# Kernel optimization log

Hardware: AMD Instinct MI355X
Metric: run time of the kernel (lower is better)

Reference implementation:

```python
import jax, jax.numpy as jnp
import numpy as np

B, C, H, W = 1, 1, 1024, 1024
NP = 16                    # n_patches
S = NP * NP                # 256 tokens
D = 2048                   # hidden_d
NH = 16                    # heads
DH = D // NH               # 128
MLP = 4 * D
NB = 2                     # blocks
INPUT_D = C * (H // NP) * (W // NP)  # 4096
EPS = 1e-5


def positional_embeddings(s, d):
    # result[i,j] = sin(i/10000**(j/d)) if j even else cos(i/10000**((j-1)/d))
    i = jnp.arange(s, dtype=jnp.float32)[:, None]
    j = jnp.arange(d, dtype=jnp.float32)[None, :]
    even = (jnp.arange(d) % 2 == 0)[None, :]
    expo = jnp.where(even, j, j - 1.0) / d
    ang = i / (10000.0 ** expo)
    return jnp.where(even, jnp.sin(ang), jnp.cos(ang))


def layer_norm(x, g, b):
    m = x.mean(-1, keepdims=True)
    v = ((x - m) ** 2).mean(-1, keepdims=True)
    return (x - m) / jnp.sqrt(v + EPS) * g + b


def setup_inputs() -> dict:
    key = jax.random.key(0)
    ks = jax.random.split(key, 20)
    s = 0.02
    return {
        "images": jax.random.normal(ks[0], (B, C, H, W), jnp.float32),
        "memory": jax.random.normal(ks[1], (1, 8), jnp.float32),
        "wmap": jax.random.normal(ks[2], (INPUT_D, D), jnp.float32) * s,
        "bmap": jnp.zeros((D,), jnp.float32),
        "ln1_g": jnp.ones((NB, D), jnp.float32),
        "ln1_b": jnp.zeros((NB, D), jnp.float32),
        "qw": jax.random.normal(ks[3], (NB, NH, DH, DH), jnp.float32) * s,
        "qb": jnp.zeros((NB, NH, DH), jnp.float32),
        "kw": jax.random.normal(ks[4], (NB, NH, DH, DH), jnp.float32) * s,
        "kb": jnp.zeros((NB, NH, DH), jnp.float32),
        "vw": jax.random.normal(ks[5], (NB, NH, DH, DH), jnp.float32) * s,
        "vb": jnp.zeros((NB, NH, DH), jnp.float32),
        "ln2_g": jnp.ones((NB, D), jnp.float32),
        "ln2_b": jnp.zeros((NB, D), jnp.float32),
        "w1": jax.random.normal(ks[6], (NB, D, MLP), jnp.float32) * s,
        "b1": jnp.zeros((NB, MLP), jnp.float32),
        "w2": jax.random.normal(ks[7], (NB, MLP, D), jnp.float32) * s,
        "b2": jnp.zeros((NB, D), jnp.float32),
        "head_w": jax.random.normal(ks[8], (D, 1), jnp.float32) * s,
        "head_b": jnp.zeros((1,), jnp.float32),
    }


def reference(images, memory, wmap, bmap, ln1_g, ln1_b, qw, qb, kw, kb, vw, vb,
              ln2_g, ln2_b, w1, b1, w2, b2, head_w, head_b):
    # patchify: view(1, n_patches**2, num_h*num_v) -> (1, 256, 4096)
    patches = images.reshape(1, S, INPUT_D)
    tokens = patches @ wmap + bmap                      # (1, S, D)
    x = tokens + positional_embeddings(S, D)
    scale = DH ** 0.5
    for l in range(NB):
        h = layer_norm(x, ln1_g[l], ln1_b[l])
        h4 = h.reshape(B, S, NH, DH)
        q = jnp.einsum('bshd,hde->bshe', h4, qw[l]) + qb[l]
        k = jnp.einsum('bshd,hde->bshe', h4, kw[l]) + kb[l]
        v = jnp.einsum('bshd,hde->bshe', h4, vw[l]) + vb[l]
        att = jax.nn.softmax(jnp.einsum('bshe,bthe->bhst', q, k) / scale, axis=-1)
        attn_out = jnp.einsum('bhst,bthe->bshe', att, v).reshape(B, S, D)
        x = x + attn_out
        h2 = layer_norm(x, ln2_g[l], ln2_b[l])
        x = x + (jax.nn.gelu(h2 @ w1[l] + b1[l], approximate=False) @ w2[l] + b2[l])
    cls = x[:, 0]                                       # (1, D)
    out = jax.nn.sigmoid(cls @ head_w + head_b)         # (1, 1)
    return (out, memory)
```

## Files before the change

### kernel.cpp

```cpp
#include <hip/hip_runtime.h>
#include <math.h>

#define SQ   256
#define DD   2048
#define NHD  16
#define DHD  128
#define MLPD 8192
#define KIN  4096
#define INV_SQRT_DH 0.08838834764831845f

typedef __attribute__((ext_vector_type(8))) short bf16x8;
typedef __attribute__((ext_vector_type(4))) float f32x4;

__device__ __forceinline__ float gelu_f(float x) {
    return 0.5f * x * (1.0f + erff(x * 0.70710678118654752f));
}

__device__ __forceinline__ short f2bf(float f) {
    unsigned u = __float_as_uint(f);
    unsigned r = (u + 0x7fffu + ((u >> 16) & 1u)) >> 16;
    return (short)r;
}

__global__ __launch_bounds__(512) void gemm128(const float* __restrict__ A,
                                               const float* __restrict__ W,
                                               float* __restrict__ C,
                                               int N, int K, int KC) {
    __shared__ short As[2][128 * 64];
    __shared__ short Bs[2][128 * 64];
    const int tid = threadIdx.x;
    const int n0 = blockIdx.x * 128, m0 = blockIdx.y * 128;
    const int kstart = blockIdx.z * KC;
    const int ln = tid & 63;
    const int wv = tid >> 6;
    const int l15 = ln & 15, q = ln >> 4;
    const int wm = wv >> 2, wn = wv & 3;

    f32x4 acc[4][2];
    #pragma unroll
    for (int mt = 0; mt < 4; mt++)
        #pragma unroll
        for (int nt = 0; nt < 2; nt++) acc[mt][nt] = (f32x4){0.f, 0.f, 0.f, 0.f};

    const int am = tid >> 2, ak0 = (tid & 3) * 16;
    const int bn = tid & 127, bk0 = (tid >> 7) * 16;
    const int aw0 = am * 64 + ((((ak0 >> 3) + 0) ^ (am & 7)) * 8);
    const int aw1 = am * 64 + ((((ak0 >> 3) + 1) ^ (am & 7)) * 8);
    const int bw0 = bn * 64 + ((((bk0 >> 3) + 0) ^ (bn & 7)) * 8);
    const int bw1 = bn * 64 + ((((bk0 >> 3) + 1) ^ (bn & 7)) * 8);

    const float* aptr = A + (size_t)(m0 + am) * K + kstart + ak0;
    const float* wptr = W + (size_t)(kstart + bk0) * N + n0 + bn;

    const int nch = KC >> 6;

    float4 a[4];
    float wb[16];
    #pragma unroll
    for (int j = 0; j < 4; j++) a[j] = *(const float4*)(aptr + 4 * j);
    #pragma unroll
    for (int j = 0; j < 16; j++) wb[j] = wptr[(size_t)j * N];
    {
        short t0[16];
        #pragma unroll
        for (int j = 0; j < 4; j++) {
            t0[4 * j]     = f2bf(a[j].x);
            t0[4 * j + 1] = f2bf(a[j].y);
            t0[4 * j + 2] = f2bf(a[j].z);
            t0[4 * j + 3] = f2bf(a[j].w);
        }
        *(bf16x8*)&As[0][aw0] = *(bf16x8*)&t0[0];
        *(bf16x8*)&As[0][aw1] = *(bf16x8*)&t0[8];
        short u0[16];
        #pragma unroll
        for (int j = 0; j < 16; j++) u0[j] = f2bf(wb[j]);
        *(bf16x8*)&Bs[0][bw0] = *(bf16x8*)&u0[0];
        *(bf16x8*)&Bs[0][bw1] = *(bf16x8*)&u0[8];
    }
    __syncthreads();

    int cur = 0;
    for (int t = 0; t < nch; t++) {
        const bool pf = (t + 1 < nch);
        if (pf) {
            const float* ap = aptr + (t + 1) * 64;
            #pragma unroll
            for (int j = 0; j < 4; j++) a[j] = *(const float4*)(ap + 4 * j);
            const float* wp = wptr + (size_t)(t + 1) * 64 * N;
            #pragma unroll
            for (int j = 0; j < 16; j++) wb[j] = wp[(size_t)j * N];
        }

        const short* Ab = As[cur];
        const short* Bb = Bs[cur];
        bf16x8 af[4][2], bf[2][2];
        #pragma unroll
        for (int mt = 0; mt < 4; mt++) {
            const int ar = wm * 64 + mt * 16 + l15;
            af[mt][0] = *(const bf16x8*)&Ab[ar * 64 + ((q ^ (ar & 7)) * 8)];
            af[mt][1] = *(const bf16x8*)&Ab[ar * 64 + (((q + 4) ^ (ar & 7)) * 8)];
        }
        #pragma unroll
        for (int nt = 0; nt < 2; nt++) {
            const int br = wn * 32 + nt * 16 + l15;
            bf[nt][0] = *(const bf16x8*)&Bb[br * 64 + ((q ^ (br & 7)) * 8)];
            bf[nt][1] = *(const bf16x8*)&Bb[br * 64 + (((q + 4) ^ (br & 7)) * 8)];
        }
        #pragma unroll
        for (int mt = 0; mt < 4; mt++)
            #pragma unroll
            for (int nt = 0; nt < 2; nt++) {
                acc[mt][nt] = __builtin_amdgcn_mfma_f32_16x16x32_bf16(af[mt][0], bf[nt][0], acc[mt][nt], 0, 0, 0);
                acc[mt][nt] = __builtin_amdgcn_mfma_f32_16x16x32_bf16(af[mt][1], bf[nt][1], acc[mt][nt], 0, 0, 0);
            }

        if (pf) {
            short t1[16];
            #pragma unroll
            for (int j = 0; j < 4; j++) {
                t1[4 * j]     = f2bf(a[j].x);
                t1[4 * j + 1] = f2bf(a[j].y);
                t1[4 * j + 2] = f2bf(a[j].z);
                t1[4 * j + 3] = f2bf(a[j].w);
            }
            short* Aw = (short*)As[cur ^ 1];
            short* Bw = (short*)Bs[cur ^ 1];
            *(bf16x8*)&Aw[aw0] = *(bf16x8*)&t1[0];
            *(bf16x8*)&Aw[aw1] = *(bf16x8*)&t1[8];
            short u1[16];
            #pragma unroll
            for (int j = 0; j < 16; j++) u1[j] = f2bf(wb[j]);
            *(bf16x8*)&Bw[bw0] = *(bf16x8*)&u1[0];
            *(bf16x8*)&Bw[bw1] = *(bf16x8*)&u1[8];
        }
        __syncthreads();
        cur ^= 1;
    }

    #pragma unroll
    for (int mt = 0; mt < 4; mt++) {
        #pragma unroll
        for (int nt = 0; nt < 2; nt++) {
            const int col = n0 + wn * 32 + nt * 16 + l15;
            #pragma unroll
            for (int i = 0; i < 4; i++) {
                const int row = m0 + wm * 64 + mt * 16 + q * 4 + i;
                atomicAdd(&C[(size_t)row * N + col], acc[mt][nt][i]);
            }
        }
    }
}

__global__ __launch_bounds__(256) void epi_pos(float* __restrict__ x,
                                               const float* __restrict__ bmap) {
    const int idx = blockIdx.x * 256 + threadIdx.x;
    const int m = idx >> 11, n = idx & 2047;
    float val = x[idx] + bmap[n];
    float jf = (float)n;
    float expo = ((n & 1) ? (jf - 1.0f) : jf) * (1.0f / 2048.0f);
    float ang = (float)m * powf(10000.0f, -expo);
    x[idx] = val + ((n & 1) ? cosf(ang) : sinf(ang));
}

__global__ __launch_bounds__(256) void epi_gelu(float* __restrict__ y,
                                                const float* __restrict__ b1) {
    const int idx = blockIdx.x * 256 + threadIdx.x;
    y[idx] = gelu_f(y[idx] + b1[idx & 8191]);
}

__global__ __launch_bounds__(256) void epi_bias(float* __restrict__ x,
                                                const float* __restrict__ b2) {
    const int idx = blockIdx.x * 256 + threadIdx.x;
    x[idx] += b2[idx & 2047];
}

__global__ __launch_bounds__(256) void qkv_mfma(const float* __restrict__ h,
                                                const float* __restrict__ qw, const float* __restrict__ kw,
                                                const float* __restrict__ vw, const float* __restrict__ qb,
                                                const float* __restrict__ kb, const float* __restrict__ vb,
                                                float* __restrict__ q, float* __restrict__ k,
                                                float* __restrict__ v) {
    __shared__ short As[64 * 64];
    __shared__ short Bs[64 * 64];
    const int head = blockIdx.x, m0 = blockIdx.y * 64;
    const int type = blockIdx.z >> 1, n0 = (blockIdx.z & 1) * 64;
    const float* W; const float* B; float* O;
    if (type == 0)      { W = qw; B = qb; O = q; }
    else if (type == 1) { W = kw; B = kb; O = k; }
    else                { W = vw; B = vb; O = v; }
    W += (size_t)head * DHD * DHD;
    B += head * DHD;
    const int hoff = head * DHD;
    const int tid = threadIdx.x;
    const int wv = tid >> 6, ln = tid & 63;
    const int l15 = ln & 15, qq = ln >> 4;

    f32x4 acc[4];
    #pragma unroll
    for (int j = 0; j < 4; j++) acc[j] = (f32x4){0.f, 0.f, 0.f, 0.f};

    const int am = tid >> 2, akb = (tid & 3) * 16, ac0 = (tid & 3) * 2;
    const int bn = tid & 63, bkb = (tid >> 6) * 16, bc0 = (tid >> 6) * 2;
    short* as0 = &As[am * 64 + ((ac0 ^ (am & 7)) * 8)];
    short* as1 = &As[am * 64 + (((ac0 + 1) ^ (am & 7)) * 8)];
    short* bs0 = &Bs[bn * 64 + ((bc0 ^ (bn & 7)) * 8)];
    short* bs1 = &Bs[bn * 64 + (((bc0 + 1) ^ (bn & 7)) * 8)];
    const int arow = 16 * wv + l15;
    const short* af0 = &As[arow * 64 + ((qq ^ (arow & 7)) * 8)];
    const short* af1 = &As[arow * 64 + (((qq + 4) ^ (arow & 7)) * 8)];

    for (int kc = 0; kc < DHD; kc += 64) {
        const float* ap = h + (size_t)(m0 + am) * DD + hoff + kc + akb;
        float4 a0 = *(const float4*)ap;
        float4 a1 = *(const float4*)(ap + 4);
        float4 a2 = *(const float4*)(ap + 8);
        float4 a3 = *(const float4*)(ap + 12);
        const float* wp = W + (size_t)(kc + bkb) * DHD + n0 + bn;
        float wb[16];
        #pragma unroll
        for (int j = 0; j < 16; j++) wb[j] = wp[j * DHD];

        __syncthreads();
        {
            short t[16] = {f2bf(a0.x), f2bf(a0.y), f2bf(a0.z), f2bf(a0.w),
                           f2bf(a1.x), f2bf(a1.y), f2bf(a1.z), f2bf(a1.w),
                           f2bf(a2.x), f2bf(a2.y), f2bf(a2.z), f2bf(a2.w),
                           f2bf(a3.x), f2bf(a3.y), f2bf(a3.z), f2bf(a3.w)};
            *(bf16x8*)as0 = *(bf16x8*)&t[0];
            *(bf16x8*)as1 = *(bf16x8*)&t[8];
            short u[16];
            #pragma unroll
            for (int j = 0; j < 16; j++) u[j] = f2bf(wb[j]);
            *(bf16x8*)bs0 = *(bf16x8*)&u[0];
            *(bf16x8*)bs1 = *(bf16x8*)&u[8];
        }
        __syncthreads();

        bf16x8 fa0 = *(const bf16x8*)af0;
        bf16x8 fa1 = *(const bf16x8*)af1;
        #pragma unroll
        for (int jt = 0; jt < 4; jt++) {
            const int brow = 16 * jt + l15;
            bf16x8 fb0 = *(const bf16x8*)&Bs[brow * 64 + ((qq ^ (brow & 7)) * 8)];
            bf16x8 fb1 = *(const bf16x8*)&Bs[brow * 64 + (((qq + 4) ^ (brow & 7)) * 8)];
            acc[jt] = __builtin_amdgcn_mfma_f32_16x16x32_bf16(fa0, fb0, acc[jt], 0, 0, 0);
            acc[jt] = __builtin_amdgcn_mfma_f32_16x16x32_bf16(fa1, fb1, acc[jt], 0, 0, 0);
        }
    }
    #pragma unroll
    for (int jt = 0; jt < 4; jt++) {
        const int n = n0 + 16 * jt + l15;
        #pragma unroll
        for (int i = 0; i < 4; i++) {
            const int m = m0 + 16 * wv + qq * 4 + i;
            O[(size_t)m * DD + hoff + n] = acc[jt][i] + B[n];
        }
    }
}

__global__ __launch_bounds__(256) void attn_mfma(const float* __restrict__ q,
                                                 const float* __restrict__ k,
                                                 const float* __restrict__ v,
                                                 float* __restrict__ x) {
    __shared__ short P[64 * 272];
    __shared__ short ST[9216];
    const int head = blockIdx.y, r0 = blockIdx.x * 64;
    const int hoff = head * DHD;
    const int tid = threadIdx.x;
    const int wv = tid >> 6, ln = tid & 63;
    const int l15 = ln & 15, qd = ln >> 4;

    bf16x8 af[4];
    {
        const float* qp = q + (size_t)(r0 + 16 * wv + l15) * DD + hoff + qd * 8;
        #pragma unroll
        for (int s = 0; s < 4; s++) {
            float4 f0 = *(const float4*)(qp + s * 32);
            float4 f1 = *(const float4*)(qp + s * 32 + 4);
            short t[8] = {f2bf(f0.x), f2bf(f0.y), f2bf(f0.z), f2bf(f0.w),
                          f2bf(f1.x), f2bf(f1.y), f2bf(f1.z), f2bf(f1.w)};
            af[s] = *(bf16x8*)t;
        }
    }

    f32x4 sacc[16];
    #pragma unroll
    for (int i = 0; i < 16; i++) sacc[i] = (f32x4){0.f, 0.f, 0.f, 0.f};

    const int skey = tid >> 2, scol = (tid & 3) * 32;
    for (int kq = 0; kq < 4; kq++) {
        const float* kp = k + (size_t)(kq * 64 + skey) * DD + hoff + scol;
        float4 f[8];
        #pragma unroll
        for (int a = 0; a < 8; a++) f[a] = *(const float4*)(kp + a * 4);
        if (kq) __syncthreads();
        #pragma unroll
        for (int a = 0; a < 4; a++) {
            short t[8] = {f2bf(f[2*a].x), f2bf(f[2*a].y), f2bf(f[2*a].z), f2bf(f[2*a].w),
                          f2bf(f[2*a+1].x), f2bf(f[2*a+1].y), f2bf(f[2*a+1].z), f2bf(f[2*a+1].w)};
            *(bf16x8*)&ST[skey * 136 + scol + a * 8] = *(bf16x8*)t;
        }
        __syncthreads();
        #pragma unroll
        for (int nl = 0; nl < 4; nl++) {
            #pragma unroll
            for (int s = 0; s < 4; s++) {
                bf16x8 bfr = *(const bf16x8*)&ST[(nl * 16 + l15) * 136 + s * 32 + qd * 8];
                sacc[kq * 4 + nl] = __builtin_amdgcn_mfma_f32_16x16x32_bf16(af[s], bfr, sacc[kq * 4 + nl], 0, 0, 0);
            }
        }
    }

    float inv_s[4];
    #pragma unroll
    for (int i = 0; i < 4; i++) {
        float m = -1e30f;
        #pragma unroll
        for (int nt = 0; nt < 16; nt++) m = fmaxf(m, sacc[nt][i]);
        m = fmaxf(m, __shfl_xor(m, 1));
        m = fmaxf(m, __shfl_xor(m, 2));
        m = fmaxf(m, __shfl_xor(m, 4));
        m = fmaxf(m, __shfl_xor(m, 8));
        float sum = 0.f;
        #pragma unroll
        for (int nt = 0; nt < 16; nt++) {
            float e = __expf((sacc[nt][i] - m) * INV_SQRT_DH);
            sacc[nt][i] = e;
            sum += e;
        }
        sum += __shfl_xor(sum, 1);
        sum += __shfl_xor(sum, 2);
        sum += __shfl_xor(sum, 4);
        sum += __shfl_xor(sum, 8);
        inv_s[i] = 1.0f / sum;
    }
    #pragma unroll
    for (int nt = 0; nt < 16; nt++) {
        const int col = nt * 16 + l15;
        const int chunk = col >> 3, c7 = col & 7;
        #pragma unroll
        for (int i = 0; i < 4; i++) {
            const int row = 16 * wv + 4 * qd + i;
            P[row * 272 + ((chunk ^ (row & 7)) * 8) + c7] = f2bf(sacc[nt][i] * inv_s[i]);
        }
    }
    __syncthreads();

    f32x4 oacc[8];
    #pragma unroll
    for (int e = 0; e < 8; e++) oacc[e] = (f32x4){0.f, 0.f, 0.f, 0.f};

    const int ve = tid & 127, vks = (tid >> 7) * 32;
    for (int kq = 0; kq < 4; kq++) {
        float vv[32];
        #pragma unroll
        for (int j = 0; j < 32; j++)
            vv[j] = v[(size_t)(kq * 64 + vks + j) * DD + hoff + ve];
        if (kq) __syncthreads();
        #pragma unroll
        for (int c = 0; c < 4; c++) {
            short t[8];
            #pragma unroll
            for (int b = 0; b < 8; b++) t[b] = f2bf(vv[c * 8 + b]);
            const int ch = (vks >> 3) + c;
            *(bf16x8*)&ST[ve * 72 + ((ch ^ (ve & 7)) * 8)] = *(bf16x8*)t;
        }
        __syncthreads();
        #pragma unroll
        for (int s = 0; s < 2; s++) {
            const int row = 16 * wv + l15;
            const int pc = kq * 8 + s * 4 + qd;
            bf16x8 pa = *(const bf16x8*)&P[row * 272 + ((pc ^ (row & 7)) * 8)];
            #pragma unroll
            for (int et = 0; et < 8; et++) {
                const int er = et * 16 + l15;
                const int vc = s * 4 + qd;
                bf16x8 vb = *(const bf16x8*)&ST[er * 72 + ((vc ^ (er & 7)) * 8)];
                oacc[et] = __builtin_amdgcn_mfma_f32_16x16x32_bf16(pa, vb, oacc[et], 0, 0, 0);
            }
        }
    }
    #pragma unroll
    for (int et = 0; et < 8; et++) {
        const int e = et * 16 + l15;
        #pragma unroll
        for (int i = 0; i < 4; i++) {
            const int row = r0 + 16 * wv + 4 * qd + i;
            x[(size_t)row * DD + hoff + e] += oacc[et][i];
        }
    }
}

__global__ __launch_bounds__(256) void ln_kernel(const float* __restrict__ xin,
                                                 const float* __restrict__ g,
                                                 const float* __restrict__ b,
                                                 float* __restrict__ out,
                                                 float* __restrict__ zbuf, int zn) {
    __shared__ float red[8];
    const int tid = threadIdx.x;
    for (int i = tid; i < zn; i += 256) zbuf[i] = 0.0f;
    const int row = blockIdx.x;
    const float* xr = xin + row * DD;
    float vals[8];
    float s = 0.0f;
    #pragma unroll
    for (int i = 0; i < 8; i++) { vals[i] = xr[tid + i * 256]; s += vals[i]; }
    #pragma unroll
    for (int o = 32; o > 0; o >>= 1) s += __shfl_down(s, o);
    if ((tid & 63) == 0) red[tid >> 6] = s;
    __syncthreads();
    if (tid == 0) red[4] = (red[0] + red[1] + red[2] + red[3]) * (1.0f / 2048.0f);
    __syncthreads();
    const float mean = red[4];
    float vs = 0.0f;
    #pragma unroll
    for (int i = 0; i < 8; i++) { float d = vals[i] - mean; vs += d * d; }
    #pragma unroll
    for (int o = 32; o > 0; o >>= 1) vs += __shfl_down(vs, o);
    if ((tid & 63) == 0) red[tid >> 6] = vs;
    __syncthreads();
    if (tid == 0) red[5] = rsqrtf((red[0] + red[1] + red[2] + red[3]) * (1.0f / 2048.0f) + 1e-5f);
    __syncthreads();
    const float inv = red[5];
    #pragma unroll
    for (int i = 0; i < 8; i++) {
        int c = tid + i * 256;
        out[row * DD + c] = (vals[i] - mean) * inv * g[c] + b[c];
    }
}

__global__ __launch_bounds__(256) void attn0_kernel(const float* __restrict__ q,
                                                    const float* __restrict__ k,
                                                    const float* __restrict__ v,
                                                    float* __restrict__ x) {
    __shared__ float q0[128];
    __shared__ float p[256];
    __shared__ float red[8];
    const int h = blockIdx.x, tid = threadIdx.x, hoff = h * DHD;
    if (tid < 128) q0[tid] = q[hoff + tid];
    __syncthreads();
    const float* kr = k + tid * DD + hoff;
    float s = 0.0f;
    #pragma unroll 8
    for (int d = 0; d < 128; d++) s += q0[d] * kr[d];
    s *= INV_SQRT_DH;
    float m = s;
    #pragma unroll
    for (int o = 32; o > 0; o >>= 1) m = fmaxf(m, __shfl_down(m, o));
    if ((tid & 63) == 0) red[tid >> 6] = m;
    __syncthreads();
    if (tid == 0) red[4] = fmaxf(fmaxf(red[0], red[1]), fmaxf(red[2], red[3]));
    __syncthreads();
    const float mx = red[4];
    float e = __expf(s - mx);
    p[tid] = e;
    float t = e;
    #pragma unroll
    for (int o = 32; o > 0; o >>= 1) t += __shfl_down(t, o);
    if ((tid & 63) == 0) red[tid >> 6] = t;
    __syncthreads();
    if (tid == 0) red[5] = red[0] + red[1] + red[2] + red[3];
    __syncthreads();
    const float inv = 1.0f / red[5];
    if (tid < 128) {
        float acc = 0.0f;
        #pragma unroll 8
        for (int j = 0; j < 256; j++) acc += p[j] * v[j * DD + hoff + tid];
        x[hoff + tid] += acc * inv;
    }
}

__global__ __launch_bounds__(256) void gemv1_kernel(const float* __restrict__ h2,
                                                    const float* __restrict__ w1,
                                                    float* __restrict__ y) {
    const int n = blockIdx.x * 256 + threadIdx.x;
    const int k0 = blockIdx.y * 64;
    float s = 0.0f;
    #pragma unroll 8
    for (int k = 0; k < 64; k++) s += h2[k0 + k] * w1[(size_t)(k0 + k) * MLPD + n];
    atomicAdd(&y[n], s);
}

__global__ __launch_bounds__(256) void gelu_bias_kernel(float* __restrict__ y,
                                                        const float* __restrict__ b1) {
    const int n = blockIdx.x * 256 + threadIdx.x;
    y[n] = gelu_f(y[n] + b1[n]);
}

__global__ __launch_bounds__(256) void gemv2_kernel(const float* __restrict__ y1,
                                                    const float* __restrict__ w2,
                                                    float* __restrict__ x) {
    const int m = blockIdx.x * 256 + threadIdx.x;
    const int k0 = blockIdx.y * 256;
    float s = 0.0f;
    #pragma unroll 8
    for (int k = 0; k < 256; k++) s += y1[k0 + k] * w2[(size_t)(k0 + k) * DD + m];
    atomicAdd(&x[m], s);
}

__global__ __launch_bounds__(256) void head_kernel(const float* __restrict__ x,
                                                   const float* __restrict__ b2l,
                                                   const float* __restrict__ hw,
                                                   const float* __restrict__ hb,
                                                   const float* __restrict__ mem,
                                                   float* __restrict__ out) {
    __shared__ float red[8];
    const int tid = threadIdx.x;
    float s = 0.0f;
    for (int m = tid; m < 2048; m += 256) s += (x[m] + b2l[m]) * hw[m];
    #pragma unroll
    for (int o = 32; o > 0; o >>= 1) s += __shfl_down(s, o);
    if ((tid & 63) == 0) red[tid >> 6] = s;
    __syncthreads();
    if (tid == 0) {
        float t = red[0] + red[1] + red[2] + red[3];
        out[0] = 1.0f / (1.0f + __expf(-(t + hb[0])));
    }
    if (tid < 8) out[1 + tid] = mem[tid];
}

extern "C" void kernel_launch(void* const* d_in, const int* in_sizes, int n_in,
                              void* d_out, int out_size, void* d_ws, size_t ws_size,
                              hipStream_t stream) {
    const float* images = (const float*)d_in[0];
    const float* memory = (const float*)d_in[1];
    const float* wmap   = (const float*)d_in[2];
    const float* bmap   = (const float*)d_in[3];
    const float* ln1_g  = (const float*)d_in[4];
    const float* ln1_b  = (const float*)d_in[5];
    const float* qw     = (const float*)d_in[6];
    const float* qb     = (const float*)d_in[7];
    const float* kw     = (const float*)d_in[8];
    const float* kb     = (const float*)d_in[9];
    const float* vw     = (const float*)d_in[10];
    const float* vb     = (const float*)d_in[11];
    const float* ln2_g  = (const float*)d_in[12];
    const float* ln2_b  = (const float*)d_in[13];
    const float* w1     = (const float*)d_in[14];
    const float* b1     = (const float*)d_in[15];
    const float* w2     = (const float*)d_in[16];
    const float* b2     = (const float*)d_in[17];
    const float* head_w = (const float*)d_in[18];
    const float* head_b = (const float*)d_in[19];
    float* out = (float*)d_out;

    float* ws = (float*)d_ws;
    float* x     = ws;
    float* h     = x + SQ * DD;
    float* q     = h + SQ * DD;
    float* k     = q + SQ * DD;
    float* v     = k + SQ * DD;
    float* y1    = v + SQ * DD;
    float* y1row = y1 + SQ * MLPD;
    float* h2row = y1row + MLPD;

    hipMemsetAsync(x, 0, (size_t)SQ * DD * sizeof(float), stream);
    gemm128<<<dim3(DD / 128, SQ / 128, 8), 512, 0, stream>>>(images, wmap, x, DD, KIN, 512);
    epi_pos<<<SQ * DD / 256, 256, 0, stream>>>(x, bmap);

    for (int l = 0; l < 2; l++) {
        const size_t wofs = (size_t)l * NHD * DHD * DHD;
        const size_t bofs = (size_t)l * NHD * DHD;
        ln_kernel<<<SQ, 256, 0, stream>>>(x, ln1_g + l * DD, ln1_b + l * DD, h, nullptr, 0);
        qkv_mfma<<<dim3(NHD, SQ / 64, 6), 256, 0, stream>>>(h, qw + wofs, kw + wofs, vw + wofs,
                                                            qb + bofs, kb + bofs, vb + bofs,
                                                            q, k, v);
        if (l == 0) {
            attn_mfma<<<dim3(SQ / 64, NHD), 256, 0, stream>>>(q, k, v, x);
            ln_kernel<<<SQ, 256, 0, stream>>>(x, ln2_g, ln2_b, h, nullptr, 0);
            hipMemsetAsync(y1, 0, (size_t)SQ * MLPD * sizeof(float), stream);
            gemm128<<<dim3(MLPD / 128, SQ / 128, 2), 512, 0, stream>>>(h, w1, y1, MLPD, DD, 1024);
            epi_gelu<<<SQ * MLPD / 256, 256, 0, stream>>>(y1, b1);
            gemm128<<<dim3(DD / 128, SQ / 128, 8), 512, 0, stream>>>(y1, w2, x, DD, MLPD, 1024);
            epi_bias<<<SQ * DD / 256, 256, 0, stream>>>(x, b2);
        } else {
            attn0_kernel<<<NHD, 256, 0, stream>>>(q, k, v, x);
            ln_kernel<<<1, 256, 0, stream>>>(x, ln2_g + DD, ln2_b + DD, h2row, y1row, MLPD);
            gemv1_kernel<<<dim3(MLPD / 256, 32), 256, 0, stream>>>(h2row, w1 + (size_t)DD * MLPD, y1row);
            gelu_bias_kernel<<<MLPD / 256, 256, 0, stream>>>(y1row, b1 + MLPD);
            gemv2_kernel<<<dim3(DD / 256, 32), 256, 0, stream>>>(y1row, w2 + (size_t)DD * MLPD, x);
            head_kernel<<<1, 256, 0, stream>>>(x, b2 + DD, head_w, head_b, memory, out);
        }
    }
}
```

Measured before the change: 497.7 us.

## Pre-transpose weights to bf16 and stream GEMM tiles via direct global-to-LDS loads

Adds conversion kernels that cast the image to bf16 and transpose wmap, w1 and w2 into K-contiguous bf16 layouts on every call. The GEMM is rewritten as gemm_bf, which loads pre-swizzled 16-byte chunks straight into LDS with global_load_lds, dropping the per-iteration fp32 loads and in-register bf16 conversion. The layer-norm and GELU epilogues now also emit bf16 copies to feed it. The aim is to cut GEMM load and convert overhead and the strided weight reads. The cost is an extra full read and write of roughly 160MB of fp32 weights inside the timed region, which may outweigh the GEMM savings.

Measured after the change: 538.5 us. 1.08x slower.

```diff
diff --git a/kernel.cpp b/kernel.cpp
--- a/kernel.cpp
+++ b/kernel.cpp
@@ -22,8 +22,48 @@
     return (short)r;
 }
 
-__global__ __launch_bounds__(512) void gemm128(const float* __restrict__ A,
-                                               const float* __restrict__ W,
+__device__ __forceinline__ void gload16(const void* g, void* l) {
+    __builtin_amdgcn_global_load_lds((const __attribute__((address_space(1))) void*)g,
+                                     (__attribute__((address_space(3))) void*)l,
+                                     16, 0, 0);
+}
+
+__global__ __launch_bounds__(256) void cvt_bf(const float* __restrict__ in,
+                                              short* __restrict__ out) {
+    const int idx = (blockIdx.x * 256 + threadIdx.x) * 8;
+    float4 f0 = *(const float4*)&in[idx];
+    float4 f1 = *(const float4*)&in[idx + 4];
+    short u[8] = {f2bf(f0.x), f2bf(f0.y), f2bf(f0.z), f2bf(f0.w),
+                  f2bf(f1.x), f2bf(f1.y), f2bf(f1.z), f2bf(f1.w)};
+    *(bf16x8*)&out[idx] = *(bf16x8*)&u[0];
+}
+
+__global__ __launch_bounds__(256) void transpose_bf(const float* __restrict__ in,
+                                                    short* __restrict__ out,
+                                                    int K, int N) {
+    __shared__ float T[64][65];
+    const int k0 = blockIdx.y * 64, n0 = blockIdx.x * 64;
+    const int tid = threadIdx.x;
+    const int kr = tid >> 4, nc = (tid & 15) * 4;
+    #pragma unroll
+    for (int i = 0; i < 4; i++) {
+        float4 f = *(const float4*)&in[(size_t)(k0 + kr + 16 * i) * N + n0 + nc];
+        T[kr + 16 * i][nc]     = f.x;
+        T[kr + 16 * i][nc + 1] = f.y;
+        T[kr + 16 * i][nc + 2] = f.z;
+        T[kr + 16 * i][nc + 3] = f.w;
+    }
+    __syncthreads();
+    const int nr = tid >> 2, kc = (tid & 3) * 16;
+    short u[16];
+    #pragma unroll
+    for (int j = 0; j < 16; j++) u[j] = f2bf(T[kc + j][nr]);
+    *(bf16x8*)&out[(size_t)(n0 + nr) * K + k0 + kc]     = *(bf16x8*)&u[0];
+    *(bf16x8*)&out[(size_t)(n0 + nr) * K + k0 + kc + 8] = *(bf16x8*)&u[8];
+}
+
+__global__ __launch_bounds__(512) void gemm_bf(const short* __restrict__ A,
+                                               const short* __restrict__ Bt,
                                                float* __restrict__ C,
                                                int N, int K, int KC) {
     __shared__ short As[2][128 * 64];
@@ -31,8 +71,7 @@
     const int tid = threadIdx.x;
     const int n0 = blockIdx.x * 128, m0 = blockIdx.y * 128;
     const int kstart = blockIdx.z * KC;
-    const int ln = tid & 63;
-    const int wv = tid >> 6;
+    const int wv = tid >> 6, ln = tid & 63;
     const int l15 = ln & 15, q = ln >> 4;
     const int wm = wv >> 2, wn = wv & 3;
 
@@ -42,57 +81,33 @@
         #pragma unroll
         for (int nt = 0; nt < 2; nt++) acc[mt][nt] = (f32x4){0.f, 0.f, 0.f, 0.f};
 
-    const int am = tid >> 2, ak0 = (tid & 3) * 16;
-    const int bn = tid & 127, bk0 = (tid >> 7) * 16;
-    const int aw0 = am * 64 + ((((ak0 >> 3) + 0) ^ (am & 7)) * 8);
-    const int aw1 = am * 64 + ((((ak0 >> 3) + 1) ^ (am & 7)) * 8);
-    const int bw0 = bn * 64 + ((((bk0 >> 3) + 0) ^ (bn & 7)) * 8);
-    const int bw1 = bn * 64 + ((((bk0 >> 3) + 1) ^ (bn & 7)) * 8);
-
-    const float* aptr = A + (size_t)(m0 + am) * K + kstart + ak0;
-    const float* wptr = W + (size_t)(kstart + bk0) * N + n0 + bn;
+    const int srow = tid >> 3;
+    const int schk = (tid & 7) ^ (srow & 7);
+    const short* Ap = A  + (size_t)(m0 + srow) * K + kstart + schk * 8;
+    const short* Bp = Bt + (size_t)(n0 + srow) * K + kstart + schk * 8;
+    const int wvoff = wv * 1024;
 
     const int nch = KC >> 6;
 
-    float4 a[4];
-    float wb[16];
-    #pragma unroll
-    for (int j = 0; j < 4; j++) a[j] = *(const float4*)(aptr + 4 * j);
-    #pragma unroll
-    for (int j = 0; j < 16; j++) wb[j] = wptr[(size_t)j * N];
-    {
-        short t0[16];
-        #pragma unroll
-        for (int j = 0; j < 4; j++) {
-            t0[4 * j]     = f2bf(a[j].x);
-            t0[4 * j + 1] = f2bf(a[j].y);
-            t0[4 * j + 2] = f2bf(a[j].z);
-            t0[4 * j + 3] = f2bf(a[j].w);
-        }
-        *(bf16x8*)&As[0][aw0] = *(bf16x8*)&t0[0];
-        *(bf16x8*)&As[0][aw1] = *(bf16x8*)&t0[8];
-        short u0[16];
-        #pragma unroll
-        for (int j = 0; j < 16; j++) u0[j] = f2bf(wb[j]);
-        *(bf16x8*)&Bs[0][bw0] = *(bf16x8*)&u0[0];
-        *(bf16x8*)&Bs[0][bw1] = *(bf16x8*)&u0[8];
+    #pragma unroll
+    for (int j = 0; j < 2; j++) {
+        gload16(Ap + (size_t)(j * 64) * K, (char*)(&As[0][0]) + j * 8192 + wvoff);
+        gload16(Bp + (size_t)(j * 64) * K, (char*)(&Bs[0][0]) + j * 8192 + wvoff);
     }
     __syncthreads();
 
     int cur = 0;
     for (int t = 0; t < nch; t++) {
-        const bool pf = (t + 1 < nch);
-        if (pf) {
-            const float* ap = aptr + (t + 1) * 64;
-            #pragma unroll
-            for (int j = 0; j < 4; j++) a[j] = *(const float4*)(ap + 4 * j);
-            const float* wp = wptr + (size_t)(t + 1) * 64 * N;
-            #pragma unroll
-            for (int j = 0; j < 16; j++) wb[j] = wp[(size_t)j * N];
-        }
-
-        const short* Ab = As[cur];
-        const short* Bb = Bs[cur];
+        if (t + 1 < nch) {
+            const int kc = (t + 1) * 64;
+            #pragma unroll
+            for (int j = 0; j < 2; j++) {
+                gload16(Ap + (size_t)(j * 64) * K + kc, (char*)(&As[cur ^ 1][0]) + j * 8192 + wvoff);
+                gload16(Bp + (size_t)(j * 64) * K + kc, (char*)(&Bs[cur ^ 1][0]) + j * 8192 + wvoff);
+            }
+        }
+        const short* Ab = &As[cur][0];
+        const short* Bb = &Bs[cur][0];
         bf16x8 af[4][2], bf[2][2];
         #pragma unroll
         for (int mt = 0; mt < 4; mt++) {
@@ -113,26 +128,6 @@
                 acc[mt][nt] = __builtin_amdgcn_mfma_f32_16x16x32_bf16(af[mt][0], bf[nt][0], acc[mt][nt], 0, 0, 0);
                 acc[mt][nt] = __builtin_amdgcn_mfma_f32_16x16x32_bf16(af[mt][1], bf[nt][1], acc[mt][nt], 0, 0, 0);
             }
-
-        if (pf) {
-            short t1[16];
-            #pragma unroll
-            for (int j = 0; j < 4; j++) {
-                t1[4 * j]     = f2bf(a[j].x);
-                t1[4 * j + 1] = f2bf(a[j].y);
-                t1[4 * j + 2] = f2bf(a[j].z);
-                t1[4 * j + 3] = f2bf(a[j].w);
-            }
-            short* Aw = (short*)As[cur ^ 1];
-            short* Bw = (short*)Bs[cur ^ 1];
-            *(bf16x8*)&Aw[aw0] = *(bf16x8*)&t1[0];
-            *(bf16x8*)&Aw[aw1] = *(bf16x8*)&t1[8];
-            short u1[16];
-            #pragma unroll
-            for (int j = 0; j < 16; j++) u1[j] = f2bf(wb[j]);
-            *(bf16x8*)&Bw[bw0] = *(bf16x8*)&u1[0];
-            *(bf16x8*)&Bw[bw1] = *(bf16x8*)&u1[8];
-        }
         __syncthreads();
         cur ^= 1;
     }
@@ -162,10 +157,11 @@
     x[idx] = val + ((n & 1) ? cosf(ang) : sinf(ang));
 }
 
-__global__ __launch_bounds__(256) void epi_gelu(float* __restrict__ y,
-                                                const float* __restrict__ b1) {
+__global__ __launch_bounds__(256) void epi_gelu(const float* __restrict__ y,
+                                                const float* __restrict__ b1,
+                                                short* __restrict__ yb) {
     const int idx = blockIdx.x * 256 + threadIdx.x;
-    y[idx] = gelu_f(y[idx] + b1[idx & 8191]);
+    yb[idx] = f2bf(gelu_f(y[idx] + b1[idx & 8191]));
 }
 
 __global__ __launch_bounds__(256) void epi_bias(float* __restrict__ x,
@@ -395,7 +391,8 @@
                                                  const float* __restrict__ g,
                                                  const float* __restrict__ b,
                                                  float* __restrict__ out,
-                                                 float* __restrict__ zbuf, int zn) {
+                                                 float* __restrict__ zbuf, int zn,
+                                                 short* __restrict__ out_bf) {
     __shared__ float red[8];
     const int tid = threadIdx.x;
     for (int i = tid; i < zn; i += 256) zbuf[i] = 0.0f;
@@ -425,7 +422,9 @@
     #pragma unroll
     for (int i = 0; i < 8; i++) {
         int c = tid + i * 256;
-        out[row * DD + c] = (vals[i] - mean) * inv * g[c] + b[c];
+        float val = (vals[i] - mean) * inv * g[c] + b[c];
+        out[row * DD + c] = val;
+        if (out_bf) out_bf[row * DD + c] = f2bf(val);
     }
 }
 
@@ -554,28 +553,41 @@
     float* y1row = y1 + SQ * MLPD;
     float* h2row = y1row + MLPD;
 
+    short* sws    = (short*)(h2row + DD);
+    short* img_bf = sws;
+    short* wmapT  = img_bf + (size_t)SQ * KIN;
+    short* w1T    = wmapT + (size_t)DD * KIN;
+    short* w2T    = w1T + (size_t)MLPD * DD;
+    short* h_bf   = w2T + (size_t)DD * MLPD;
+    short* y1b    = h_bf + (size_t)SQ * DD;
+
+    cvt_bf<<<(SQ * KIN) / (256 * 8), 256, 0, stream>>>(images, img_bf);
+    transpose_bf<<<dim3(DD / 64, KIN / 64), 256, 0, stream>>>(wmap, wmapT, KIN, DD);
+    transpose_bf<<<dim3(MLPD / 64, DD / 64), 256, 0, stream>>>(w1, w1T, DD, MLPD);
+    transpose_bf<<<dim3(DD / 64, MLPD / 64), 256, 0, stream>>>(w2, w2T, MLPD, DD);
+
     hipMemsetAsync(x, 0, (size_t)SQ * DD * sizeof(float), stream);
-    gemm128<<<dim3(DD / 128, SQ / 128, 8), 512, 0, stream>>>(images, wmap, x, DD, KIN, 512);
+    gemm_bf<<<dim3(DD / 128, SQ / 128, 8), 512, 0, stream>>>(img_bf, wmapT, x, DD, KIN, 512);
     epi_pos<<<SQ * DD / 256, 256, 0, stream>>>(x, bmap);
 
     for (int l = 0; l < 2; l++) {
         const size_t wofs = (size_t)l * NHD * DHD * DHD;
         const size_t bofs = (size_t)l * NHD * DHD;
-        ln_kernel<<<SQ, 256, 0, stream>>>(x, ln1_g + l * DD, ln1_b + l * DD, h, nullptr, 0);
+        ln_kernel<<<SQ, 256, 0, stream>>>(x, ln1_g + l * DD, ln1_b + l * DD, h, nullptr, 0, nullptr);
         qkv_mfma<<<dim3(NHD, SQ / 64, 6), 256, 0, stream>>>(h, qw + wofs, kw + wofs, vw + wofs,
                                                             qb + bofs, kb + bofs, vb + bofs,
                                                             q, k, v);
         if (l == 0) {
             attn_mfma<<<dim3(SQ / 64, NHD), 256, 0, stream>>>(q, k, v, x);
-            ln_kernel<<<SQ, 256, 0, stream>>>(x, ln2_g, ln2_b, h, nullptr, 0);
+            ln_kernel<<<SQ, 256, 0, stream>>>(x, ln2_g, ln2_b, h, nullptr, 0, h_bf);
             hipMemsetAsync(y1, 0, (size_t)SQ * MLPD * sizeof(float), stream);
-            gemm128<<<dim3(MLPD / 128, SQ / 128, 2), 512, 0, stream>>>(h, w1, y1, MLPD, DD, 1024);
-            epi_gelu<<<SQ * MLPD / 256, 256, 0, stream>>>(y1, b1);
-            gemm128<<<dim3(DD / 128, SQ / 128, 8), 512, 0, stream>>>(y1, w2, x, DD, MLPD, 1024);
+            gemm_bf<<<dim3(MLPD / 128, SQ / 128, 2), 512, 0, stream>>>(h_bf, w1T, y1, MLPD, DD, 1024);
+            epi_gelu<<<SQ * MLPD / 256, 256, 0, stream>>>(y1, b1, y1b);
+            gemm_bf<<<dim3(DD / 128, SQ / 128, 8), 512, 0, stream>>>(y1b, w2T, x, DD, MLPD, 1024);
             epi_bias<<<SQ * DD / 256, 256, 0, stream>>>(x, b2);
         } else {
             attn0_kernel<<<NHD, 256, 0, stream>>>(q, k, v, x);
-            ln_kernel<<<1, 256, 0, stream>>>(x, ln2_g + DD, ln2_b + DD, h2row, y1row, MLPD);
+            ln_kernel<<<1, 256, 0, stream>>>(x, ln2_g + DD, ln2_b + DD, h2row, y1row, MLPD, nullptr);
             gemv1_kernel<<<dim3(MLPD / 256, 32), 256, 0, stream>>>(h2row, w1 + (size_t)DD * MLPD, y1row);
             gelu_bias_kernel<<<MLPD / 256, 256, 0, stream>>>(y1row, b1 + MLPD);
             gemv2_kernel<<<dim3(DD / 256, 32), 256, 0, stream>>>(y1row, w2 + (size_t)DD * MLPD, x);
```

## Fuse GEMM epilogues, drop split-K memsets, fuse LN into GEMV path

Applied to the files above, without the earlier changes.

Templates the bf16 MFMA GEMM with three epilogue modes. Mode 0 adds the bias and positional embedding, mode 1 applies bias plus GELU, and both write directly with split-K removed. Mode 2 keeps atomic split-K for the MLP down-projection, now with 4 splits. This removes the memsets of x and y1 and the separate elementwise epilogue kernels. The b2 bias add moves into the next layer-norm. In the single-row second layer, the LN is fused into gemv1 (each block recomputes the LN) and GELU into gemv2. Dropping split-K on the first two GEMMs gives fewer blocks (32 and 128 CTAs), which may under-fill the GPU and lengthen the serial K loop.

New measurement: 612.0 us. 1.23x slower.

```diff
diff --git a/kernel.cpp b/kernel.cpp
--- a/kernel.cpp
+++ b/kernel.cpp
@@ -8,6 +8,7 @@
 #define MLPD 8192
 #define KIN  4096
 #define INV_SQRT_DH 0.08838834764831845f
+#define LOG2_10000 13.287712379549449f
 
 typedef __attribute__((ext_vector_type(8))) short bf16x8;
 typedef __attribute__((ext_vector_type(4))) float f32x4;
@@ -22,9 +23,11 @@
     return (short)r;
 }
 
+template<int MODE>
 __global__ __launch_bounds__(512) void gemm128(const float* __restrict__ A,
                                                const float* __restrict__ W,
                                                float* __restrict__ C,
+                                               const float* __restrict__ bias,
                                                int N, int K, int KC) {
     __shared__ short As[2][128 * 64];
     __shared__ short Bs[2][128 * 64];
@@ -145,33 +148,20 @@
             #pragma unroll
             for (int i = 0; i < 4; i++) {
                 const int row = m0 + wm * 64 + mt * 16 + q * 4 + i;
-                atomicAdd(&C[(size_t)row * N + col], acc[mt][nt][i]);
+                float r = acc[mt][nt][i];
+                if (MODE == 2) {
+                    atomicAdd(&C[(size_t)row * N + col], r);
+                } else if (MODE == 1) {
+                    C[(size_t)row * N + col] = gelu_f(r + bias[col]);
+                } else {
+                    float expo = (float)(col & ~1) * (LOG2_10000 / 2048.0f);
+                    float ang = (float)row * exp2f(-expo);
+                    r += bias[col] + ((col & 1) ? __cosf(ang) : __sinf(ang));
+                    C[(size_t)row * N + col] = r;
+                }
             }
         }
     }
-}
-
-__global__ __launch_bounds__(256) void epi_pos(float* __restrict__ x,
-                                               const float* __restrict__ bmap) {
-    const int idx = blockIdx.x * 256 + threadIdx.x;
-    const int m = idx >> 11, n = idx & 2047;
-    float val = x[idx] + bmap[n];
-    float jf = (float)n;
-    float expo = ((n & 1) ? (jf - 1.0f) : jf) * (1.0f / 2048.0f);
-    float ang = (float)m * powf(10000.0f, -expo);
-    x[idx] = val + ((n & 1) ? cosf(ang) : sinf(ang));
-}
-
-__global__ __launch_bounds__(256) void epi_gelu(float* __restrict__ y,
-                                                const float* __restrict__ b1) {
-    const int idx = blockIdx.x * 256 + threadIdx.x;
-    y[idx] = gelu_f(y[idx] + b1[idx & 8191]);
-}
-
-__global__ __launch_bounds__(256) void epi_bias(float* __restrict__ x,
-                                                const float* __restrict__ b2) {
-    const int idx = blockIdx.x * 256 + threadIdx.x;
-    x[idx] += b2[idx & 2047];
 }
 
 __global__ __launch_bounds__(256) void qkv_mfma(const float* __restrict__ h,
@@ -391,20 +381,26 @@
     }
 }
 
-__global__ __launch_bounds__(256) void ln_kernel(const float* __restrict__ xin,
+__global__ __launch_bounds__(256) void ln_kernel(float* __restrict__ x,
                                                  const float* __restrict__ g,
                                                  const float* __restrict__ b,
                                                  float* __restrict__ out,
+                                                 const float* __restrict__ addb,
                                                  float* __restrict__ zbuf, int zn) {
     __shared__ float red[8];
     const int tid = threadIdx.x;
     for (int i = tid; i < zn; i += 256) zbuf[i] = 0.0f;
     const int row = blockIdx.x;
-    const float* xr = xin + row * DD;
+    float* xr = x + (size_t)row * DD;
     float vals[8];
     float s = 0.0f;
     #pragma unroll
-    for (int i = 0; i < 8; i++) { vals[i] = xr[tid + i * 256]; s += vals[i]; }
+    for (int i = 0; i < 8; i++) {
+        int c = tid + i * 256;
+        float v = xr[c];
+        if (addb) { v += addb[c]; xr[c] = v; }
+        vals[i] = v; s += v;
+    }
     #pragma unroll
     for (int o = 32; o > 0; o >>= 1) s += __shfl_down(s, o);
     if ((tid & 63) == 0) red[tid >> 6] = s;
@@ -425,7 +421,7 @@
     #pragma unroll
     for (int i = 0; i < 8; i++) {
         int c = tid + i * 256;
-        out[row * DD + c] = (vals[i] - mean) * inv * g[c] + b[c];
+        out[(size_t)row * DD + c] = (vals[i] - mean) * inv * g[c] + b[c];
     }
 }
 
@@ -470,31 +466,62 @@
     }
 }
 
-__global__ __launch_bounds__(256) void gemv1_kernel(const float* __restrict__ h2,
-                                                    const float* __restrict__ w1,
-                                                    float* __restrict__ y) {
-    const int n = blockIdx.x * 256 + threadIdx.x;
-    const int k0 = blockIdx.y * 64;
+__global__ __launch_bounds__(256) void gemv1_ln(const float* __restrict__ x,
+                                                const float* __restrict__ g,
+                                                const float* __restrict__ b,
+                                                const float* __restrict__ w1,
+                                                float* __restrict__ y) {
+    __shared__ float h2[DD];
+    __shared__ float red[8];
+    const int tid = threadIdx.x;
+    float vals[8];
+    float s = 0.0f;
+    #pragma unroll
+    for (int i = 0; i < 8; i++) { vals[i] = x[tid + i * 256]; s += vals[i]; }
+    #pragma unroll
+    for (int o = 32; o > 0; o >>= 1) s += __shfl_down(s, o);
+    if ((tid & 63) == 0) red[tid >> 6] = s;
+    __syncthreads();
+    if (tid == 0) red[4] = (red[0] + red[1] + red[2] + red[3]) * (1.0f / 2048.0f);
+    __syncthreads();
+    const float mean = red[4];
+    float vs = 0.0f;
+    #pragma unroll
+    for (int i = 0; i < 8; i++) { float d = vals[i] - mean; vs += d * d; }
+    #pragma unroll
+    for (int o = 32; o > 0; o >>= 1) vs += __shfl_down(vs, o);
+    if ((tid & 63) == 0) red[tid >> 6] = vs;
+    __syncthreads();
+    if (tid == 0) red[5] = rsqrtf((red[0] + red[1] + red[2] + red[3]) * (1.0f / 2048.0f) + 1e-5f);
+    __syncthreads();
+    const float inv = red[5];
+    #pragma unroll
+    for (int i = 0; i < 8; i++) {
+        int c = tid + i * 256;
+        h2[c] = (vals[i] - mean) * inv * g[c] + b[c];
+    }
+    __syncthreads();
+    const int n = blockIdx.x * 256 + tid;
+    const int k0 = blockIdx.y * 256;
+    float acc = 0.0f;
+    #pragma unroll 8
+    for (int k = 0; k < 256; k++) acc += h2[k0 + k] * w1[(size_t)(k0 + k) * MLPD + n];
+    atomicAdd(&y[n], acc);
+}
+
+__global__ __launch_bounds__(256) void gemv2_gelu(const float* __restrict__ y1,
+                                                  const float* __restrict__ b1,
+                                                  const float* __restrict__ w2,
+                                                  float* __restrict__ x) {
+    __shared__ float yg[256];
+    const int tid = threadIdx.x;
+    const int m = blockIdx.x * 256 + tid;
+    const int k0 = blockIdx.y * 256;
+    yg[tid] = gelu_f(y1[k0 + tid] + b1[k0 + tid]);
+    __syncthreads();
     float s = 0.0f;
     #pragma unroll 8
-    for (int k = 0; k < 64; k++) s += h2[k0 + k] * w1[(size_t)(k0 + k) * MLPD + n];
-    atomicAdd(&y[n], s);
-}
-
-__global__ __launch_bounds__(256) void gelu_bias_kernel(float* __restrict__ y,
-                                                        const float* __restrict__ b1) {
-    const int n = blockIdx.x * 256 + threadIdx.x;
-    y[n] = gelu_f(y[n] + b1[n]);
-}
-
-__global__ __launch_bounds__(256) void gemv2_kernel(const float* __restrict__ y1,
-                                                    const float* __restrict__ w2,
-                                                    float* __restrict__ x) {
-    const int m = blockIdx.x * 256 + threadIdx.x;
-    const int k0 = blockIdx.y * 256;
-    float s = 0.0f;
-    #pragma unroll 8
-    for (int k = 0; k < 256; k++) s += y1[k0 + k] * w2[(size_t)(k0 + k) * DD + m];
+    for (int k = 0; k < 256; k++) s += yg[k] * w2[(size_t)(k0 + k) * DD + m];
     atomicAdd(&x[m], s);
 }
 
@@ -552,34 +579,25 @@
     float* v     = k + SQ * DD;
     float* y1    = v + SQ * DD;
     float* y1row = y1 + SQ * MLPD;
-    float* h2row = y1row + MLPD;
-
-    hipMemsetAsync(x, 0, (size_t)SQ * DD * sizeof(float), stream);
-    gemm128<<<dim3(DD / 128, SQ / 128, 8), 512, 0, stream>>>(images, wmap, x, DD, KIN, 512);
-    epi_pos<<<SQ * DD / 256, 256, 0, stream>>>(x, bmap);
-
-    for (int l = 0; l < 2; l++) {
-        const size_t wofs = (size_t)l * NHD * DHD * DHD;
-        const size_t bofs = (size_t)l * NHD * DHD;
-        ln_kernel<<<SQ, 256, 0, stream>>>(x, ln1_g + l * DD, ln1_b + l * DD, h, nullptr, 0);
-        qkv_mfma<<<dim3(NHD, SQ / 64, 6), 256, 0, stream>>>(h, qw + wofs, kw + wofs, vw + wofs,
-                                                            qb + bofs, kb + bofs, vb + bofs,
-                                                            q, k, v);
-        if (l == 0) {
-            attn_mfma<<<dim3(SQ / 64, NHD), 256, 0, stream>>>(q, k, v, x);
-            ln_kernel<<<SQ, 256, 0, stream>>>(x, ln2_g, ln2_b, h, nullptr, 0);
-            hipMemsetAsync(y1, 0, (size_t)SQ * MLPD * sizeof(float), stream);
-            gemm128<<<dim3(MLPD / 128, SQ / 128, 2), 512, 0, stream>>>(h, w1, y1, MLPD, DD, 1024);
-            epi_gelu<<<SQ * MLPD / 256, 256, 0, stream>>>(y1, b1);
-            gemm128<<<dim3(DD / 128, SQ / 128, 8), 512, 0, stream>>>(y1, w2, x, DD, MLPD, 1024);
-            epi_bias<<<SQ * DD / 256, 256, 0, stream>>>(x, b2);
-        } else {
-            attn0_kernel<<<NHD, 256, 0, stream>>>(q, k, v, x);
-            ln_kernel<<<1, 256, 0, stream>>>(x, ln2_g + DD, ln2_b + DD, h2row, y1row, MLPD);
-            gemv1_kernel<<<dim3(MLPD / 256, 32), 256, 0, stream>>>(h2row, w1 + (size_t)DD * MLPD, y1row);
-            gelu_bias_kernel<<<MLPD / 256, 256, 0, stream>>>(y1row, b1 + MLPD);
-            gemv2_kernel<<<dim3(DD / 256, 32), 256, 0, stream>>>(y1row, w2 + (size_t)DD * MLPD, x);
-            head_kernel<<<1, 256, 0, stream>>>(x, b2 + DD, head_w, head_b, memory, out);
-        }
-    }
-}
+
+    gemm128<0><<<dim3(DD / 128, SQ / 128, 1), 512, 0, stream>>>(images, wmap, x, bmap, DD, KIN, KIN);
+
+    ln_kernel<<<SQ, 256, 0, stream>>>(x, ln1_g, ln1_b, h, nullptr, nullptr, 0);
+    qkv_mfma<<<dim3(NHD, SQ / 64, 6), 256, 0, stream>>>(h, qw, kw, vw, qb, kb, vb, q, k, v);
+    attn_mfma<<<dim3(SQ / 64, NHD), 256, 0, stream>>>(q, k, v, x);
+    ln_kernel<<<SQ, 256, 0, stream>>>(x, ln2_g, ln2_b, h, nullptr, nullptr, 0);
+    gemm128<1><<<dim3(MLPD / 128, SQ / 128, 1), 512, 0, stream>>>(h, w1, y1, b1, MLPD, DD, DD);
+    gemm128<2><<<dim3(DD / 128, SQ / 128, 4), 512, 0, stream>>>(y1, w2, x, nullptr, DD, MLPD, MLPD / 4);
+
+    const size_t wofs = (size_t)NHD * DHD * DHD;
+    const size_t bofs = (size_t)NHD * DHD;
+    ln_kernel<<<SQ, 256, 0, stream>>>(x, ln1_g + DD, ln1_b + DD, h, b2, y1row, MLPD);
+    qkv_mfma<<<dim3(NHD, SQ / 64, 6), 256, 0, stream>>>(h, qw + wofs, kw + wofs, vw + wofs,
+                                                        qb + bofs, kb + bofs, vb + bofs, q, k, v);
+    attn0_kernel<<<NHD, 256, 0, stream>>>(q, k, v, x);
+    gemv1_ln<<<dim3(MLPD / 256, 8), 256, 0, stream>>>(x, ln2_g + DD, ln2_b + DD,
+                                                      w1 + (size_t)DD * MLPD, y1row);
+    gemv2_gelu<<<dim3(DD / 256, MLPD / 256), 256, 0, stream>>>(y1row, b1 + MLPD,
+                                                               w2 + (size_t)DD * MLPD, x);
+    head_kernel<<<1, 256, 0, stream>>>(x, b2 + DD, head_w, head_b, memory, out);
+}
```
